# Kernel optimization log

Measured on AMD Instinct MI355X. Metric: run time of the kernel, lower is better.

## Reference

```python
import jax, jax.numpy as jnp
import numpy as np
from jax import lax

L, B, S, D, V, NL = 64, 32, 64, 512, 32000, 2


def setup_inputs() -> dict:
    key = jax.random.key(0)
    ks = jax.random.split(key, 9)
    sd = 1.0 / np.sqrt(D)
    return {
        "rnn_input": jax.random.randint(ks[0], (L, B), 0, V),
        "last_hidden": jax.random.normal(ks[1], (NL, B, D), jnp.float32),
        "encoder_outputs": jax.random.normal(ks[2], (S, B, D), jnp.float32),
        "embed_table": jax.random.normal(ks[3], (V, D), jnp.float32) * sd,
        "sru_W": jax.random.normal(ks[4], (NL, D, 3 * D), jnp.float32) * sd,
        "sru_b": jax.random.normal(ks[5], (NL, 2 * D), jnp.float32) * 0.01,
        "attn_W": jax.random.normal(ks[6], (2 * D, D), jnp.float32) * sd,
        "out_W": jax.random.normal(ks[7], (D, V), jnp.float32) * sd,
        "out_b": jax.random.normal(ks[8], (V,), jnp.float32) * 0.01,
    }


def _sru_layer(x, c0, W, b):
    # x: [L,B,D] layer input, c0: [B,D], W: [D,3D], b: [2D]
    U = jnp.einsum('lbd,de->lbe', x, W)          # [L,B,3D]
    z, fp, rp = jnp.split(U, 3, axis=-1)          # candidate, forget, reset pre-acts
    bf, br = jnp.split(b, 2)
    f = jax.nn.sigmoid(fp + bf)
    r = jax.nn.sigmoid(rp + br)

    def step(c, inp):
        f_t, z_t = inp
        c = f_t * c + (1.0 - f_t) * z_t
        return c, c

    c_last, c_seq = lax.scan(step, c0, (f, z))    # c_seq: [L,B,D]
    h = r * jnp.tanh(c_seq) + (1.0 - r) * x       # highway (n_in == n_out)
    return h, c_last


def reference(rnn_input, last_hidden, encoder_outputs, embed_table, sru_W, sru_b, attn_W, out_W, out_b):
    x = embed_table[rnn_input]                    # [L,B,D]
    finals = []
    for l in range(NL):                           # small fixed layer loop
        x, c_last = _sru_layer(x, last_hidden[l], sru_W[l], sru_b[l])
        finals.append(c_last)
    hidden = jnp.stack(finals, axis=0)            # [NL,B,D]

    q = jnp.transpose(x, (1, 0, 2))               # [B,L,D]
    mem = jnp.transpose(encoder_outputs, (1, 0, 2))  # [B,S,D]
    scores = jnp.einsum('bld,bsd->bls', q, mem)   # dot attention
    align = jax.nn.softmax(scores, axis=-1)
    ctx = jnp.einsum('bls,bsd->bld', align, mem)
    attn_h = jnp.tanh(jnp.concatenate([ctx, q], axis=-1) @ attn_W)  # [B,L,D]
    output = attn_h @ out_W + out_b               # [B,L,V]
    return output, hidden
```

## Files before the change

kernel.cpp:

```cpp
#include <hip/hip_runtime.h>
#include <hip/hip_bf16.h>

#define L_ 64
#define B_ 32
#define S_ 64
#define D_ 512
#define V_ 32000
#define NL_ 2

typedef __attribute__((ext_vector_type(8))) short bf16x8;
typedef __attribute__((ext_vector_type(4))) float f32x4;

static __device__ __forceinline__ short f2bf(float f) {
  union { float f; unsigned u; } x; x.f = f;
  unsigned r = (x.u + 0x7FFFu + ((x.u >> 16) & 1u)) >> 16;
  return (short)r;
}

#define GLOAD_LDS16(g, l)                                                     \
  __builtin_amdgcn_global_load_lds(                                           \
      (const __attribute__((address_space(1))) void*)(g),                     \
      (__attribute__((address_space(3))) void*)(l), 16, 0, 0)

__global__ void prep_kernel(const float* __restrict__ sruW, const float* __restrict__ attnW,
                            const float* __restrict__ outW, const int* __restrict__ tok,
                            const float* __restrict__ tab,
                            short* __restrict__ WTs, short* __restrict__ WTa,
                            short* __restrict__ WTo,
                            float* __restrict__ xf, short* __restrict__ xb) {
  int bid = blockIdx.x;
  int tx = threadIdx.x, ty = threadIdx.y;
  __shared__ float tile[32][33];
  if (bid < 18048) {
    const float* in;
    short* out;
    int K, N, bx, by;
    if (bid < 1536) {
      int l = (bid >= 768) ? 1 : 0;
      int r = bid - l * 768;
      bx = r % 48; by = r / 48; K = 512; N = 1536;
      in = sruW + (size_t)l * 512 * 1536;
      out = WTs + (size_t)l * 1536 * 512;
    } else if (bid < 2048) {
      int r = bid - 1536;
      bx = r % 16; by = r / 16; K = 1024; N = 512;
      in = attnW; out = WTa;
    } else {
      int r = bid - 2048;
      bx = r % 1000; by = r / 1000; K = 512; N = 32000;
      in = outW; out = WTo;
    }
    int x = bx * 32 + tx;
    int y0 = by * 32;
    for (int j = ty; j < 32; j += 8) {
      int y = y0 + j;
      tile[j][tx] = (x < N && y < K) ? in[(size_t)y * N + x] : 0.f;
    }
    __syncthreads();
    int xo = y0 + tx;
    int yo0 = bx * 32;
    for (int j = ty; j < 32; j += 8) {
      int yo = yo0 + j;
      if (yo < N && xo < K) out[(size_t)yo * K + xo] = f2bf(tile[tx][j]);
    }
  } else {
    int i = (bid - 18048) * 256 + ty * 32 + tx;
    int d = i & (D_ - 1);
    int lb = i >> 9;
    float v = tab[(size_t)tok[lb] * D_ + d];
    xf[i] = v;
    xb[i] = f2bf(v);
  }
}

template <int BMt, int BNt, int WM, int WN, int MODE>
__global__ __launch_bounds__(256) void gemm_t(
    const short* __restrict__ A, const short* __restrict__ BT,
    void* __restrict__ Cptr, const float* __restrict__ bias,
    int M, int N, int K, int nbm) {
  constexpr int MI = BMt / WM / 16;
  constexpr int NI = BNt / WN / 16;
  constexpr int ACH = BMt / 8;
  constexpr int NCH = (BMt + BNt) / 8;
  constexpr int CPW = NCH / 4;

  const int nwg = gridDim.x;
  const int qc = nwg >> 3;
  const int bid = blockIdx.x;
  const int wg = (bid & 7) * qc + (bid >> 3);
  const int bm = wg % nbm;
  const int bn = wg / nbm;

  __shared__ __align__(16) short la[2][BMt * 64];
  __shared__ __align__(16) short lb[2][BNt * 64];
  const int tid = threadIdx.x;
  const int wave = tid >> 6, lane = tid & 63;
  const int wm = (wave / WN) * (BMt / WM);
  const int wn = (wave % WN) * (BNt / WN);

  f32x4 acc[MI][NI] = {};

  const int lrow = lane >> 3;
  const int lslot = lane & 7;
  const short* Abase = A + (size_t)(bm * BMt) * K;
  const short* Bbase = BT + (size_t)(bn * BNt) * K;

  auto stage = [&](int buf, int k0) {
#pragma unroll
    for (int c = 0; c < CPW; ++c) {
      int chunk = wave * CPW + c;
      if (chunk < ACH) {
        int row = chunk * 8 + lrow;
        int slot = lslot ^ (row & 7);
        GLOAD_LDS16(Abase + (size_t)row * K + k0 + slot * 8, &la[buf][chunk * 512]);
      } else {
        int bc = chunk - ACH;
        int row = bc * 8 + lrow;
        int slot = lslot ^ (row & 7);
        GLOAD_LDS16(Bbase + (size_t)row * K + k0 + slot * 8, &lb[buf][bc * 512]);
      }
    }
  };

  stage(0, 0);
  __syncthreads();

  const int nt = K / 64;
  int cur = 0;
  for (int t = 0; t < nt; ++t) {
    if (t + 1 < nt) stage(cur ^ 1, (t + 1) * 64);
#pragma unroll
    for (int kk = 0; kk < 2; ++kk) {
      bf16x8 af[MI], bfr[NI];
#pragma unroll
      for (int mi = 0; mi < MI; ++mi) {
        int row = wm + mi * 16 + (lane & 15);
        int slot = (kk * 4 + (lane >> 4)) ^ (row & 7);
        af[mi] = *(const bf16x8*)&la[cur][row * 64 + slot * 8];
      }
#pragma unroll
      for (int ni = 0; ni < NI; ++ni) {
        int row = wn + ni * 16 + (lane & 15);
        int slot = (kk * 4 + (lane >> 4)) ^ (row & 7);
        bfr[ni] = *(const bf16x8*)&lb[cur][row * 64 + slot * 8];
      }
#pragma unroll
      for (int mi = 0; mi < MI; ++mi)
#pragma unroll
        for (int ni = 0; ni < NI; ++ni)
          acc[mi][ni] = __builtin_amdgcn_mfma_f32_16x16x32_bf16(
              af[mi], bfr[ni], acc[mi][ni], 0, 0, 0);
    }
    __syncthreads();
    cur ^= 1;
  }

  const int cl = lane & 15;
  const int rl = (lane >> 4) * 4;
#pragma unroll
  for (int mi = 0; mi < MI; ++mi) {
#pragma unroll
    for (int ni = 0; ni < NI; ++ni) {
      int c = bn * BNt + wn + ni * 16 + cl;
      int r0 = bm * BMt + wm + mi * 16 + rl;
#pragma unroll
      for (int j = 0; j < 4; ++j) {
        int r = r0 + j;
        float v = acc[mi][ni][j];
        if (MODE == 0) {
          ((float*)Cptr)[(size_t)r * N + c] = v;
        } else if (MODE == 1) {
          ((short*)Cptr)[(size_t)r * N + c] = f2bf(tanhf(v));
        } else if (MODE == 3) {
          if (c >= 512) v = 1.f / (1.f + expf(-(v + bias[c - 512])));
          ((float*)Cptr)[(size_t)r * N + c] = v;
        }
      }
    }
  }
}

template <int MODE>
__global__ __launch_bounds__(256, 4) void gemm_s(
    const short* __restrict__ A, const short* __restrict__ BT,
    void* __restrict__ Cptr, const float* __restrict__ bias,
    int M, int N, int K, int nbm) {
  const int nwg = gridDim.x;
  const int qc = nwg >> 3;
  const int bid = blockIdx.x;
  const int wg = (bid & 7) * qc + (bid >> 3);
  const int bm = wg % nbm;
  const int bn = wg / nbm;

  __shared__ __align__(16) short la[128 * 64];
  __shared__ __align__(16) short lb[128 * 64];
  const int tid = threadIdx.x;
  const int wave = tid >> 6, lane = tid & 63;
  const int wm = (wave >> 1) * 64, wn = (wave & 1) * 64;

  f32x4 acc[4][4] = {};

  const int lrow = lane >> 3;
  const int lslot = lane & 7;
  const short* Abase = A + (size_t)(bm * 128) * K;
  const short* Bbase = BT + (size_t)(bn * 128) * K;

  const int nt = K / 64;
  for (int t = 0; t < nt; ++t) {
    const int k0 = t * 64;
#pragma unroll
    for (int c = 0; c < 4; ++c) {
      int chunk = wave * 4 + c;
      int row = chunk * 8 + lrow;
      int slot = lslot ^ (row & 7);
      GLOAD_LDS16(Abase + (size_t)row * K + k0 + slot * 8, &la[chunk * 512]);
      GLOAD_LDS16(Bbase + (size_t)row * K + k0 + slot * 8, &lb[chunk * 512]);
    }
    __syncthreads();
#pragma unroll
    for (int kk = 0; kk < 2; ++kk) {
      bf16x8 af[4], bfr[4];
#pragma unroll
      for (int mi = 0; mi < 4; ++mi) {
        int row = wm + mi * 16 + (lane & 15);
        int slot = (kk * 4 + (lane >> 4)) ^ (row & 7);
        af[mi] = *(const bf16x8*)&la[row * 64 + slot * 8];
      }
#pragma unroll
      for (int ni = 0; ni < 4; ++ni) {
        int row = wn + ni * 16 + (lane & 15);
        int slot = (kk * 4 + (lane >> 4)) ^ (row & 7);
        bfr[ni] = *(const bf16x8*)&lb[row * 64 + slot * 8];
      }
#pragma unroll
      for (int mi = 0; mi < 4; ++mi)
#pragma unroll
        for (int ni = 0; ni < 4; ++ni)
          acc[mi][ni] = __builtin_amdgcn_mfma_f32_16x16x32_bf16(
              af[mi], bfr[ni], acc[mi][ni], 0, 0, 0);
    }
    __syncthreads();
  }

  const int cl = lane & 15;
  const int rl = (lane >> 4) * 4;
#pragma unroll
  for (int mi = 0; mi < 4; ++mi) {
#pragma unroll
    for (int ni = 0; ni < 4; ++ni) {
      int c = bn * 128 + wn + ni * 16 + cl;
      int r0 = bm * 128 + wm + mi * 16 + rl;
      float bs = (MODE == 2) ? bias[c] : 0.f;
#pragma unroll
      for (int j = 0; j < 4; ++j) {
        int r = r0 + j;
        float v = acc[mi][ni][j];
        if (MODE == 2) {
          int b = r & 31, l = r >> 5;
          ((float*)Cptr)[(size_t)(b * L_ + l) * N + c] = v + bs;
        } else {
          ((float*)Cptr)[(size_t)r * N + c] = v;
        }
      }
    }
  }
}

__global__ void sru_scan_kernel(const float* __restrict__ U,
                                const float* __restrict__ xin, const float* __restrict__ c0,
                                float* __restrict__ hf, short* __restrict__ hb,
                                float* __restrict__ clast) {
  int idx = blockIdx.x * 64 + threadIdx.x;
  int b = idx >> 9, d = idx & 511;
  float c = c0[idx];
  const float* Ub = U + (size_t)b * 1536 + d;
  const float* Xb = xin + (size_t)b * 512 + d;

  for (int l0 = 0; l0 < L_; l0 += 8) {
    float z[8], f[8], r[8], xv[8];
#pragma unroll
    for (int j = 0; j < 8; ++j) {
      size_t u = (size_t)(l0 + j) * B_ * 1536;
      z[j] = Ub[u];
      f[j] = Ub[u + 512];
      r[j] = Ub[u + 1024];
      xv[j] = Xb[(size_t)(l0 + j) * B_ * 512];
    }
#pragma unroll
    for (int j = 0; j < 8; ++j) {
      c = f[j] * c + (1.f - f[j]) * z[j];
      float h = r[j] * tanhf(c) + (1.f - r[j]) * xv[j];
      size_t o = ((size_t)(l0 + j) * B_ + b) * 512 + d;
      hf[o] = h;
      hb[o] = f2bf(h);
    }
  }
  clast[idx] = c;
}

__global__ __launch_bounds__(256) void attn_fused_kernel(
    const float* __restrict__ x, const float* __restrict__ enc,
    const short* __restrict__ xq, short* __restrict__ cat) {
  __shared__ float q[512];
  __shared__ float al[64];
  int r = blockIdx.x;
  int b = r & (B_ - 1);
  int tid = threadIdx.x;
  int wave = tid >> 6, lane = tid & 63;
  for (int d = tid; d < 512; d += 256) {
    q[d] = x[(size_t)r * 512 + d];
    cat[(size_t)r * 1024 + 512 + d] = xq[(size_t)r * 512 + d];
  }
  __syncthreads();
#pragma unroll
  for (int si = 0; si < 16; ++si) {
    int s = wave * 16 + si;
    const float* m = enc + ((size_t)s * B_ + b) * 512;
    float a = 0.f;
#pragma unroll
    for (int k = 0; k < 8; ++k) a += q[lane + k * 64] * m[lane + k * 64];
    for (int o = 32; o > 0; o >>= 1) a += __shfl_xor(a, o);
    if (lane == 0) al[s] = a;
  }
  __syncthreads();
  if (tid < 64) {
    float v = al[tid];
    float mx = v;
    for (int o = 32; o > 0; o >>= 1) mx = fmaxf(mx, __shfl_xor(mx, o));
    float e = expf(v - mx);
    float sm = e;
    for (int o = 32; o > 0; o >>= 1) sm += __shfl_xor(sm, o);
    al[tid] = e / sm;
  }
  __syncthreads();
  for (int d = tid; d < 512; d += 256) {
    float acc = 0.f;
#pragma unroll 16
    for (int s = 0; s < S_; ++s) acc += al[s] * enc[((size_t)s * B_ + b) * 512 + d];
    cat[(size_t)r * 1024 + d] = f2bf(acc);
  }
}

extern "C" void kernel_launch(void* const* d_in, const int* in_sizes, int n_in,
                              void* d_out, int out_size, void* d_ws, size_t ws_size,
                              hipStream_t stream) {
  const int* rnn = (const int*)d_in[0];
  const float* h0 = (const float*)d_in[1];
  const float* enc = (const float*)d_in[2];
  const float* tab = (const float*)d_in[3];
  const float* sruW = (const float*)d_in[4];
  const float* srub = (const float*)d_in[5];
  const float* attnW = (const float*)d_in[6];
  const float* outW = (const float*)d_in[7];
  const float* outb = (const float*)d_in[8];
  float* out = (float*)d_out;

  char* ws = (char*)d_ws;
  size_t off = 0;
  auto alloc = [&](size_t bytes) {
    char* p = ws + off;
    off += (bytes + 255) & ~(size_t)255;
    return p;
  };
  float* xf = (float*)alloc(4ull * 2048 * 512);
  float* xf2 = (float*)alloc(4ull * 2048 * 512);
  short* xb = (short*)alloc(2ull * 2048 * 512);
  float* U = (float*)alloc(4ull * 2048 * 1536);
  short* WTs = (short*)alloc(2ull * 2 * 1536 * 512);
  short* WTa = (short*)alloc(2ull * 512 * 1024);
  short* WTo = (short*)alloc(2ull * 32000 * 512);
  short* cat = (short*)alloc(2ull * 2048 * 1024);
  short* ah = (short*)alloc(2ull * 2048 * 512);

  prep_kernel<<<22144, dim3(32, 8), 0, stream>>>(sruW, attnW, outW, rnn, tab,
                                                 WTs, WTa, WTo, xf, xb);

  float* hidden_out = out + (size_t)B_ * L_ * V_;

  gemm_t<64, 128, 1, 4, 3><<<384, 256, 0, stream>>>(xb, WTs, U, srub, 2048, 1536, 512, 32);
  sru_scan_kernel<<<256, 64, 0, stream>>>(U, xf, h0, xf2, xb, hidden_out);
  gemm_t<64, 128, 1, 4, 3><<<384, 256, 0, stream>>>(xb, WTs + 1536 * 512, U, srub + 1024,
                                                    2048, 1536, 512, 32);
  sru_scan_kernel<<<256, 64, 0, stream>>>(U, xf2, h0 + B_ * D_, xf, xb,
                                          hidden_out + B_ * D_);

  attn_fused_kernel<<<2048, 256, 0, stream>>>(xf, enc, xb, cat);

  gemm_t<64, 64, 2, 2, 1><<<256, 256, 0, stream>>>(cat, WTa, ah, nullptr, 2048, 512, 1024, 32);
  gemm_s<2><<<4000, 256, 0, stream>>>(ah, WTo, out, outb, 2048, 32000, 512, 16);
}
```

Before: 230.9 us.

## Replace sequential SRU scan with warp-shuffle parallel prefix scan over time

The SRU recurrence is rewritten as a parallel affine prefix scan. Each block stages a 64-timestep by 64-feature tile of z/f/r/x into shared memory, and each wave computes the scan across the 64 timesteps with shuffle-up steps, one lane per timestep. This replaces the 64-step serial dependency chain per thread, run with only 256 single-wave blocks, with log-depth scans and four times as many threads. The cost is extra multiplies, shared-memory traffic and a change in floating-point summation order.

```diff
diff --git a/kernel.cpp b/kernel.cpp
--- a/kernel.cpp
+++ b/kernel.cpp
@@ -266,36 +266,58 @@
   }
 }
 
-__global__ void sru_scan_kernel(const float* __restrict__ U,
-                                const float* __restrict__ xin, const float* __restrict__ c0,
-                                float* __restrict__ hf, short* __restrict__ hb,
-                                float* __restrict__ clast) {
-  int idx = blockIdx.x * 64 + threadIdx.x;
-  int b = idx >> 9, d = idx & 511;
-  float c = c0[idx];
-  const float* Ub = U + (size_t)b * 1536 + d;
-  const float* Xb = xin + (size_t)b * 512 + d;
-
-  for (int l0 = 0; l0 < L_; l0 += 8) {
-    float z[8], f[8], r[8], xv[8];
-#pragma unroll
-    for (int j = 0; j < 8; ++j) {
-      size_t u = (size_t)(l0 + j) * B_ * 1536;
-      z[j] = Ub[u];
-      f[j] = Ub[u + 512];
-      r[j] = Ub[u + 1024];
-      xv[j] = Xb[(size_t)(l0 + j) * B_ * 512];
-    }
-#pragma unroll
-    for (int j = 0; j < 8; ++j) {
-      c = f[j] * c + (1.f - f[j]) * z[j];
-      float h = r[j] * tanhf(c) + (1.f - r[j]) * xv[j];
-      size_t o = ((size_t)(l0 + j) * B_ + b) * 512 + d;
-      hf[o] = h;
-      hb[o] = f2bf(h);
-    }
-  }
-  clast[idx] = c;
+__global__ __launch_bounds__(256) void sru_scan_kernel(
+    const float* __restrict__ U, const float* __restrict__ xin,
+    const float* __restrict__ c0, float* __restrict__ hf,
+    short* __restrict__ hb, float* __restrict__ clast) {
+  __shared__ float zs[64][65], fs[64][65], rs[64][65], xs[64][65];
+  int bid = blockIdx.x;
+  int b = bid >> 3;
+  int d0 = (bid & 7) * 64;
+  int tid = threadIdx.x;
+  int wave = tid >> 6, lane = tid & 63;
+
+  for (int it = 0; it < 16; ++it) {
+    int idx = it * 256 + tid;
+    int l = idx >> 6, dp = idx & 63;
+    size_t ub = ((size_t)(l * B_ + b)) * 1536 + d0 + dp;
+    zs[l][dp] = U[ub];
+    fs[l][dp] = U[ub + 512];
+    rs[l][dp] = U[ub + 1024];
+    xs[l][dp] = xin[((size_t)(l * B_ + b)) * 512 + d0 + dp];
+  }
+  __syncthreads();
+
+  for (int dd = 0; dd < 16; ++dd) {
+    int dp = wave * 16 + dd;
+    float f = fs[lane][dp];
+    float A = f;
+    float Bv = (1.f - f) * zs[lane][dp];
+#pragma unroll
+    for (int s = 1; s < 64; s <<= 1) {
+      float pa = __shfl_up(A, s);
+      float pb = __shfl_up(Bv, s);
+      if (lane >= s) {
+        Bv = A * pb + Bv;
+        A = A * pa;
+      }
+    }
+    float c = A * c0[b * 512 + d0 + dp] + Bv;
+    float r = rs[lane][dp];
+    float h = r * tanhf(c) + (1.f - r) * xs[lane][dp];
+    zs[lane][dp] = h;
+    if (lane == 63) clast[b * 512 + d0 + dp] = c;
+  }
+  __syncthreads();
+
+  for (int it = 0; it < 16; ++it) {
+    int idx = it * 256 + tid;
+    int l = idx >> 6, dp = idx & 63;
+    float h = zs[l][dp];
+    size_t o = ((size_t)(l * B_ + b)) * 512 + d0 + dp;
+    hf[o] = h;
+    hb[o] = f2bf(h);
+  }
 }
 
 __global__ __launch_bounds__(256) void attn_fused_kernel(
@@ -378,11 +400,11 @@
   float* hidden_out = out + (size_t)B_ * L_ * V_;
 
   gemm_t<64, 128, 1, 4, 3><<<384, 256, 0, stream>>>(xb, WTs, U, srub, 2048, 1536, 512, 32);
-  sru_scan_kernel<<<256, 64, 0, stream>>>(U, xf, h0, xf2, xb, hidden_out);
+  sru_scan_kernel<<<256, 256, 0, stream>>>(U, xf, h0, xf2, xb, hidden_out);
   gemm_t<64, 128, 1, 4, 3><<<384, 256, 0, stream>>>(xb, WTs + 1536 * 512, U, srub + 1024,
                                                     2048, 1536, 512, 32);
-  sru_scan_kernel<<<256, 64, 0, stream>>>(U, xf2, h0 + B_ * D_, xf, xb,
-                                          hidden_out + B_ * D_);
+  sru_scan_kernel<<<256, 256, 0, stream>>>(U, xf2, h0 + B_ * D_, xf, xb,
+                                           hidden_out + B_ * D_);
 
   attn_fused_kernel<<<2048, 256, 0, stream>>>(xf, enc, xb, cat);
 
```

New measurement: 234.1 us. About the same (+1.4%).
